# Kernel tuning notes

Hardware: AMD Instinct MI355X
Metric: run time of the kernel (lower is better)

## Reference

```python
import jax, jax.numpy as jnp
import numpy as np

B, C, H, W = 4, 128, 256, 256
N, NPOS, KS = 4000, 8, 3
CH = 2 * NPOS  # mask=False -> 2*n_pos offset channels


def setup_inputs() -> dict:
    key = jax.random.key(0)
    ks = jax.random.split(key, 8)
    x = jax.random.normal(ks[0], (B, C, H, W), jnp.float32)
    keypoints = jax.random.uniform(ks[1], (B, N, 2), jnp.float32) * 2.0 - 1.0  # [-1,1]
    w1 = jax.random.normal(ks[2], (CH, C, KS, KS), jnp.float32) * 0.05  # offset conv 3x3
    b1 = jnp.zeros((CH,), jnp.float32)
    w2 = jax.random.normal(ks[3], (CH, CH), jnp.float32) * 0.05        # offset conv 1x1
    b2 = jnp.zeros((CH,), jnp.float32)
    wsf = jax.random.normal(ks[4], (C, C), jnp.float32) * 0.05         # sf_conv 1x1 no bias
    agg_weights = jax.random.uniform(ks[5], (NPOS, C, C), jnp.float32)  # torch.rand init
    return {"x": x, "keypoints": keypoints, "w1": w1, "b1": b1, "w2": w2,
            "b2": b2, "wsf": wsf, "agg_weights": agg_weights}


def _bilinear_sample(img, px, py):
    """grid_sample(mode=bilinear, align_corners=True, padding=zeros) at pixel coords.
    img: (C,H,W); px,py: (M,). Returns (C,M)."""
    c, h, w = img.shape
    x0f = jnp.floor(px); y0f = jnp.floor(py)
    x0 = x0f.astype(jnp.int32); y0 = y0f.astype(jnp.int32)
    wx1 = px - x0f; wx0 = 1.0 - wx1
    wy1 = py - y0f; wy0 = 1.0 - wy1

    def tap(xi, yi, wgt):
        valid = ((xi >= 0) & (xi < w) & (yi >= 0) & (yi < h)).astype(img.dtype)
        v = img[:, jnp.clip(yi, 0, h - 1), jnp.clip(xi, 0, w - 1)]  # (C,M)
        return v * (wgt * valid)

    return (tap(x0, y0, wx0 * wy0) + tap(x0 + 1, y0, wx1 * wy0)
            + tap(x0, y0 + 1, wx0 * wy1) + tap(x0 + 1, y0 + 1, wx1 * wy1))


def _per_image(xi, kpts, w1, b1, w2, b2, wsf, agg_weights):
    wh = jnp.array([W - 1.0, H - 1.0], xi.dtype)
    max_offset = max(H, W) / 4.0
    kwh = (kpts / 2.0 + 0.5) * wh                      # (N,2) pixel coords, >=0
    rc = kwh.astype(jnp.int32)                          # .long() trunc (positive)
    corner = jnp.trunc(rc.astype(jnp.float32) - KS / 2.0 + 1.0).astype(jnp.int32)
    cx = jnp.clip(corner[:, 0], 0, W - 1 - KS)
    cy = jnp.clip(corner[:, 1], 0, H - 1 - KS)
    ar = jnp.arange(KS)
    # patch[n,c,a,b] = xi[c, cy_n+a, cx_n+b]
    patch = xi[:, (cy[:, None] + ar)[:, :, None], (cx[:, None] + ar)[:, None, :]]  # (C,N,KS,KS)
    patch = patch.transpose(1, 0, 2, 3)                 # (N,C,KS,KS)
    # offset network: 3x3 conv (valid) on 3x3 patch == full contraction, then ReLU, 1x1 conv
    h1 = jax.nn.relu(jnp.einsum('nchw,ochw->no', patch, w1) + b1)
    off = jnp.clip(h1 @ w2.T + b2, -max_offset, max_offset)  # (N, 2*NPOS)
    off = off.reshape(-1, 2, NPOS).transpose(0, 2, 1)        # (N,NPOS,2)
    # deform sampling positions; torch normalizes then grid_sample(align_corners=True)
    # maps exactly back to pixel coords, so sample at pixel coords directly
    pos = kwh[:, None, :] + off                              # (N,NPOS,2)
    feats = _bilinear_sample(xi, pos[..., 0].reshape(-1), pos[..., 1].reshape(-1))  # (C,N*NPOS)
    feats = feats.reshape(C, -1, NPOS).transpose(1, 0, 2)    # (N,C,NPOS)
    feats = jax.nn.selu(jnp.einsum('ncp,dc->ndp', feats, wsf))
    descs = jnp.einsum('ncp,pcd->nd', feats, agg_weights)    # (N,C)
    descs = descs / jnp.maximum(jnp.linalg.norm(descs, axis=1, keepdims=True), 1e-12)
    return descs, off


def reference(x, keypoints, w1, b1, w2, b2, wsf, agg_weights):
    f = jax.vmap(lambda xi, k: _per_image(xi, k, w1, b1, w2, b2, wsf, agg_weights))
    descriptors, offsets = f(x, keypoints)
    return descriptors, offsets  # (B,N,C), (B,N,NPOS,2)
```

## Files before the change

### kernel.cpp

```cpp
#include <hip/hip_runtime.h>
#include <math.h>

#define BB 4
#define CC 128
#define HH 256
#define WW 256
#define NN 4000
#define NPOS 8
#define KS 3
#define HWSZ (HH*WW)

#define SELU_ALPHA 1.6732632423543772f
#define SELU_SCALE 1.0507009873554805f
#define MAX_OFFSET 64.0f

typedef unsigned short ushort_t;
typedef short short8 __attribute__((ext_vector_type(8)));
typedef float f32x4 __attribute__((ext_vector_type(4)));
typedef unsigned short ushort4_t __attribute__((ext_vector_type(4)));
typedef unsigned short ushort8_t __attribute__((ext_vector_type(8)));

#define XT_ELEMS    ((size_t)BB*HH*WW*CC)
#define WSFBF_ELEMS ((size_t)CC*CC)
#define AGGT_ELEMS  ((size_t)NPOS*CC*CC)
#define W1T_ELEMS   ((size_t)16*CC*9)
#define NKP         (BB*NN)
#define NSORTBLK    ((NKP + 255) / 256)
#define HISTU_ELEMS ((size_t)NSORTBLK*256)
#define WS_NEEDED   ((XT_ELEMS+WSFBF_ELEMS+AGGT_ELEMS+W1T_ELEMS+HISTU_ELEMS)*sizeof(ushort_t) \
                     + (2*(size_t)NKP)*sizeof(int))

__device__ __forceinline__ ushort_t f2bf(float f) {
    unsigned u = __builtin_bit_cast(unsigned, f);
    unsigned r = (u + 0x7FFFu + ((u >> 16) & 1u)) >> 16;
    return (ushort_t)r;
}
__device__ __forceinline__ float bf2f(ushort_t u) {
    return __builtin_bit_cast(float, ((unsigned)u) << 16);
}

__device__ __forceinline__ int kp_bucket(const float* __restrict__ kpts, int i) {
    float kx = kpts[(size_t)i * 2 + 0];
    float ky = kpts[(size_t)i * 2 + 1];
    float kwx = (kx * 0.5f + 0.5f) * (float)(WW - 1);
    float kwy = (ky * 0.5f + 0.5f) * (float)(HH - 1);
    int rcx = (int)kwx, rcy = (int)kwy;
    int b = i / NN;
    return b * 64 + ((rcy >> 5) << 3) + (rcx >> 5);
}

__global__ __launch_bounds__(256) void ksort_hist(
    const float* __restrict__ kpts, int* __restrict__ bucket_of,
    ushort_t* __restrict__ hist63u)
{
    const int t  = threadIdx.x;
    const int hb = blockIdx.x;
    __shared__ int lh[256];
    lh[t] = 0;
    __syncthreads();
    int i = hb * 256 + t;
    if (i < NKP) {
        int bk = kp_bucket(kpts, i);
        int rank = atomicAdd(&lh[bk], 1);
        bucket_of[i] = (bk << 8) | rank;
    }
    __syncthreads();
    hist63u[hb * 256 + t] = (ushort_t)lh[t];
}

__global__ __launch_bounds__(256) void ksort_scatter(
    const int* __restrict__ bucket_of, const ushort_t* __restrict__ hist63u,
    int* __restrict__ perm)
{
    const int t = threadIdx.x;
    const int j = blockIdx.x;
    __shared__ ushort_t hall[NSORTBLK * 256];
    __shared__ int si[768];

    const int* src = (const int*)hist63u;
    int* dst = (int*)hall;
    for (int v = t; v < (NSORTBLK * 256) / 2; v += 256) dst[v] = src[v];
    __syncthreads();

    int tot = 0, before = 0;
    #pragma unroll
    for (int b2 = 0; b2 < NSORTBLK; ++b2) {
        int h = hall[b2 * 256 + t];
        tot += h;
        if (b2 < j) before += h;
    }
    si[t] = tot;
    __syncthreads();
    #pragma unroll
    for (int off = 1; off < 256; off <<= 1) {
        int add = (t >= off) ? si[t - off] : 0;
        __syncthreads();
        si[t] += add;
        __syncthreads();
    }
    int sb_t = si[t] - tot;
    __syncthreads();
    si[256 + t] = sb_t;
    si[512 + t] = before;
    __syncthreads();
    int i = j * 256 + t;
    if (i < NKP) {
        int v = bucket_of[i];
        int bk = v >> 8, rank = v & 255;
        perm[si[256 + bk] + si[512 + bk] + rank] = i;
    }
}

__global__ __launch_bounds__(256) void k0p(
    const float* __restrict__ x, ushort_t* __restrict__ xt,
    const float* __restrict__ wsf, const float* __restrict__ agg,
    const float* __restrict__ w1,
    ushort_t* __restrict__ wsf_bf, ushort_t* __restrict__ aggT_bf,
    ushort_t* __restrict__ w1t_bf)
{
    int blk = blockIdx.x;
    const int t = threadIdx.x;
    if (blk >= BB * HH * 4) {
        int i = (blk - BB * HH * 4) * 256 + t;
        if (i < CC * CC) wsf_bf[i] = f2bf(wsf[i]);
        if (i < NPOS * CC * CC) {
            int p = i >> 14, d = (i >> 7) & 127, c = i & 127;
            aggT_bf[i] = f2bf(agg[(p << 14) + (c << 7) + d]);
        }
        if (i < 16 * 1152) {
            int o = i / 1152, e = i - o * 1152, k = e >> 7, c = e & 127;
            w1t_bf[i] = f2bf(w1[o * 1152 + c * 9 + k]);
        }
        return;
    }
    int xc = blk & 3, y = (blk >> 2) & 255, b = blk >> 10;
    int x0 = xc * 64;
    __shared__ ushort_t lds[64][136];

    const float* xb = x + (size_t)b * CC * HWSZ + (size_t)y * WW + x0;
    for (int v = t; v < 2048; v += 256) {
        int c = v >> 4, xo4 = v & 15;
        float4 val = *(const float4*)(xb + (size_t)c * HWSZ + xo4 * 4);
        lds[xo4*4+0][c] = f2bf(val.x);
        lds[xo4*4+1][c] = f2bf(val.y);
        lds[xo4*4+2][c] = f2bf(val.z);
        lds[xo4*4+3][c] = f2bf(val.w);
    }
    __syncthreads();
    ushort_t* outb = xt + ((size_t)b * HWSZ + (size_t)y * WW + x0) * CC;
    for (int v = t; v < 2048; v += 256) {
        int xo = v >> 5, c4 = v & 31;
        ushort4_t val;
        val[0] = lds[xo][c4*4+0];
        val[1] = lds[xo][c4*4+1];
        val[2] = lds[xo][c4*4+2];
        val[3] = lds[xo][c4*4+3];
        *(ushort4_t*)(outb + (size_t)xo * CC + c4 * 4) = val;
    }
}

__global__ __launch_bounds__(256, 2) void k14_fused(
    const ushort_t* __restrict__ xt, const float* __restrict__ kpts,
    const ushort_t* __restrict__ w1t_bf, const float* __restrict__ b1,
    const float* __restrict__ w2, const float* __restrict__ b2,
    const ushort_t* __restrict__ wsf_bf, const ushort_t* __restrict__ aggT_bf,
    const int* __restrict__ perm,
    float* __restrict__ out_desc, float* __restrict__ out_off)
{
    const int t    = threadIdx.x;
    const int wv   = t >> 6;
    const int lane = t & 63;
    const int m    = lane & 15;
    const int q    = lane >> 4;
    const int bid  = blockIdx.x;
    const int sb   = (bid & 7) * ((BB * NN / 16) >> 3) + (bid >> 3);
    const int n0   = sb * 16;

    __shared__ ushort_t fg[CC * CC];
    union PT {
        float partials[4][16][16];
        struct { int tapoff[128][4]; float tapw[128][4]; } tp;
    };
    __shared__ PT    upt;
    __shared__ float h1f[16][17];
    __shared__ float offs[16][16];
    __shared__ float kw[16][2];
    __shared__ int   cxy[16][2];
    __shared__ int   kpi[16];
    __shared__ float wsum[4][16];
    __shared__ float rn[16];

    if (t < 16) {
        int kidx = perm[n0 + t];
        kpi[t] = kidx;
        float kx = kpts[(size_t)kidx * 2 + 0];
        float ky = kpts[(size_t)kidx * 2 + 1];
        float kwx = (kx * 0.5f + 0.5f) * (float)(WW - 1);
        float kwy = (ky * 0.5f + 0.5f) * (float)(HH - 1);
        kw[t][0] = kwx; kw[t][1] = kwy;
        int rcx = (int)kwx, rcy = (int)kwy;
        int cx = (int)truncf((float)rcx - 0.5f);
        int cy = (int)truncf((float)rcy - 0.5f);
        cxy[t][0] = min(max(cx, 0), WW - 1 - KS);
        cxy[t][1] = min(max(cy, 0), HH - 1 - KS);
    }
    __syncthreads();
    const int b = kpi[0] / NN;
    const ushort_t* xb = xt + (size_t)b * HWSZ * CC;

    {
        int px0 = cxy[m][0], py0 = cxy[m][1];
        const ushort_t* brow = w1t_bf + m * 1152 + wv * 288 + q * 8;
        short8 a0, a1, a2, a3, a4, a5, a6, a7, a8;
        #define LOAD_A(idx, dst) { \
            int e = wv * 288 + (idx) * 32 + q * 8; \
            int k = e >> 7, c = e & 127; \
            int kd = k / 3, kx2 = k - kd * 3; \
            dst = *(const short8*)(xb + ((size_t)((py0 + kd) * WW + px0 + kx2)) * CC + c); }
        LOAD_A(0, a0) LOAD_A(1, a1) LOAD_A(2, a2) LOAD_A(3, a3) LOAD_A(4, a4)
        LOAD_A(5, a5) LOAD_A(6, a6) LOAD_A(7, a7) LOAD_A(8, a8)
        #undef LOAD_A
        f32x4 hacc = {0.f, 0.f, 0.f, 0.f};
        #define MF(idx, areg) { \
            short8 bfr = *(const short8*)(brow + (idx) * 32); \
            hacc = __builtin_amdgcn_mfma_f32_16x16x32_bf16(areg, bfr, hacc, 0, 0, 0); }
        MF(0, a0) MF(1, a1) MF(2, a2) MF(3, a3) MF(4, a4)
        MF(5, a5) MF(6, a6) MF(7, a7) MF(8, a8)
        #undef MF
        #pragma unroll
        for (int r = 0; r < 4; ++r) upt.partials[wv][q * 4 + r][m] = hacc[r];
    }
    __syncthreads();
    {
        int kp = t >> 4, o = t & 15;
        float h = upt.partials[0][kp][o] + upt.partials[1][kp][o]
                + upt.partials[2][kp][o] + upt.partials[3][kp][o] + b1[o];
        h1f[kp][o] = fmaxf(h, 0.f);
    }
    __syncthreads();
    {
        int kp = t >> 4, j = t & 15;
        float s = b2[j];
        #pragma unroll
        for (int o = 0; o < 16; ++o) s += h1f[kp][o] * w2[j * 16 + o];
        s = fminf(fmaxf(s, -MAX_OFFSET), MAX_OFFSET);
        offs[kp][j] = s;
        int p = j & 7, comp = j >> 3;
        out_off[((size_t)kpi[kp] * 8 + p) * 2 + comp] = s;
    }
    __syncthreads();

    if (t < 128) {
        int kp = t >> 3, p = t & 7;
        float px = kw[kp][0] + offs[kp][p];
        float py = kw[kp][1] + offs[kp][8 + p];
        float x0f = floorf(px), y0f = floorf(py);
        int x0 = (int)x0f, y0 = (int)y0f;
        float wx1 = px - x0f, wx0 = 1.f - wx1;
        float wy1 = py - y0f, wy0 = 1.f - wy1;
        int x0c = min(max(x0, 0), WW - 1);
        int x1c = min(max(x0 + 1, 0), WW - 1);
        int y0c = min(max(y0, 0), HH - 1);
        int y1c = min(max(y0 + 1, 0), HH - 1);
        float vx0 = (x0 >= 0 && x0 < WW) ? 1.f : 0.f;
        float vx1 = (x0 + 1 >= 0 && x0 + 1 < WW) ? 1.f : 0.f;
        float vy0 = (y0 >= 0 && y0 < HH) ? 1.f : 0.f;
        float vy1 = (y0 + 1 >= 0 && y0 + 1 < HH) ? 1.f : 0.f;
        upt.tp.tapoff[t][0] = (y0c * WW + x0c) * CC;
        upt.tp.tapoff[t][1] = (y0c * WW + x1c) * CC;
        upt.tp.tapoff[t][2] = (y1c * WW + x0c) * CC;
        upt.tp.tapoff[t][3] = (y1c * WW + x1c) * CC;
        upt.tp.tapw[t][0] = wx0 * wy0 * vx0 * vy0;
        upt.tp.tapw[t][1] = wx1 * wy0 * vx1 * vy0;
        upt.tp.tapw[t][2] = wx0 * wy1 * vx0 * vy1;
        upt.tp.tapw[t][3] = wx1 * wy1 * vx1 * vy1;
    }
    __syncthreads();

    {
        const int grp = t >> 4;
        const int cl  = t & 15;
        #pragma unroll
        for (int half = 0; half < 2; ++half) {
            ushort8_t tv0[4], tv1[4], tv2[4], tv3[4];
            float4 twv[4];
            #pragma unroll
            for (int i = 0; i < 4; ++i) {
                int pair = (half * 4 + i) * 16 + grp;
                const int* to = upt.tp.tapoff[pair];
                twv[i] = *(const float4*)upt.tp.tapw[pair];
                tv0[i] = *(const ushort8_t*)(xb + to[0] + cl * 8);
                tv1[i] = *(const ushort8_t*)(xb + to[1] + cl * 8);
                tv2[i] = *(const ushort8_t*)(xb + to[2] + cl * 8);
                tv3[i] = *(const ushort8_t*)(xb + to[3] + cl * 8);
            }
            #pragma unroll
            for (int i = 0; i < 4; ++i) {
                int pair = (half * 4 + i) * 16 + grp;
                float w00 = twv[i].x, w01 = twv[i].y, w10 = twv[i].z, w11 = twv[i].w;
                ushort8_t out;
                #pragma unroll
                for (int j = 0; j < 8; ++j) {
                    float v = bf2f(tv0[i][j]) * w00;
                    v += bf2f(tv1[i][j]) * w01;
                    v += bf2f(tv2[i][j]) * w10;
                    v += bf2f(tv3[i][j]) * w11;
                    out[j] = f2bf(v);
                }
                unsigned byte = ((unsigned)(pair * 256 + cl * 16))
                              ^ (((unsigned)(pair & 7)) << 4);
                *(ushort8_t*)((char*)fg + byte) = out;
            }
        }
    }
    __syncthreads();

    for (int rti = 0; rti < 2; ++rti) {
        int rt = wv * 2 + rti;
        int r  = rt * 16 + m;
        unsigned key = ((unsigned)(r & 7)) << 4;
        short8 afr[4];
        #pragma unroll
        for (int kk = 0; kk < 4; ++kk) {
            unsigned byte = ((unsigned)(r * 256 + q * 16 + kk * 64)) ^ key;
            afr[kk] = *(const short8*)((const char*)fg + byte);
        }
        for (int ct = 0; ct < 8; ++ct) {
            const ushort_t* brow = wsf_bf + (ct * 16 + m) * CC + q * 8;
            f32x4 acc = {0.f, 0.f, 0.f, 0.f};
            #pragma unroll
            for (int kk = 0; kk < 4; ++kk) {
                short8 bfr = *(const short8*)(brow + kk * 32);
                acc = __builtin_amdgcn_mfma_f32_16x16x32_bf16(afr[kk], bfr, acc, 0, 0, 0);
            }
            #pragma unroll
            for (int rr = 0; rr < 4; ++rr) {
                float s = acc[rr];
                s = (s > 0.f) ? (SELU_SCALE * s)
                              : (SELU_SCALE * SELU_ALPHA * (expf(s) - 1.f));
                int row = rt * 16 + q * 4 + rr;
                int col = ct * 16 + m;
                unsigned byte = ((unsigned)(row * 256 + col * 2))
                              ^ (((unsigned)((row >> 3) & 7)) << 4);
                *(ushort_t*)((char*)fg + byte) = f2bf(s);
            }
        }
    }
    __syncthreads();

    f32x4 acc2[2];
    acc2[0] = (f32x4){0.f, 0.f, 0.f, 0.f};
    acc2[1] = (f32x4){0.f, 0.f, 0.f, 0.f};
    const int ctbase = wv * 2;
    for (int kk = 0; kk < 32; ++kk) {
        int p    = kk >> 2;
        int rowA = m * 8 + p;
        unsigned byte = ((unsigned)(rowA * 256 + (kk & 3) * 64 + q * 16))
                      ^ (((unsigned)((rowA >> 3) & 7)) << 4);
        short8 afr = *(const short8*)((const char*)fg + byte);
        #pragma unroll
        for (int i = 0; i < 2; ++i) {
            int ct = ctbase + i;
            const ushort_t* brow = aggT_bf + (size_t)(p * CC + ct * 16 + m) * CC
                                 + (kk & 3) * 32 + q * 8;
            short8 bfr = *(const short8*)brow;
            acc2[i] = __builtin_amdgcn_mfma_f32_16x16x32_bf16(afr, bfr, acc2[i], 0, 0, 0);
        }
    }

    {
        float ss[4];
        #pragma unroll
        for (int rr = 0; rr < 4; ++rr)
            ss[rr] = acc2[0][rr] * acc2[0][rr] + acc2[1][rr] * acc2[1][rr];
        #pragma unroll
        for (int mask = 1; mask <= 8; mask <<= 1) {
            #pragma unroll
            for (int rr = 0; rr < 4; ++rr) ss[rr] += __shfl_xor(ss[rr], mask);
        }
        if (m == 0) {
            #pragma unroll
            for (int rr = 0; rr < 4; ++rr) wsum[wv][q * 4 + rr] = ss[rr];
        }
    }
    __syncthreads();
    if (t < 16) {
        float tot = wsum[0][t] + wsum[1][t] + wsum[2][t] + wsum[3][t];
        rn[t] = 1.0f / fmaxf(sqrtf(tot), 1e-12f);
    }
    __syncthreads();
    {
        #pragma unroll
        for (int i = 0; i < 2; ++i) {
            int col = (ctbase + i) * 16 + m;
            #pragma unroll
            for (int rr = 0; rr < 4; ++rr) {
                int n = q * 4 + rr;
                out_desc[(size_t)kpi[n] * CC + col] = acc2[i][rr] * rn[n];
            }
        }
    }
}

__global__ __launch_bounds__(256, 4) void sddh_baseline(
    const float* __restrict__ x, const float* __restrict__ keypoints,
    const float* __restrict__ w1, const float* __restrict__ b1,
    const float* __restrict__ w2, const float* __restrict__ b2,
    const float* __restrict__ wsf, const float* __restrict__ agg,
    float* __restrict__ out_desc, float* __restrict__ out_off)
{
    const int bn = blockIdx.x;
    const int b  = bn / NN;
    const int t  = threadIdx.x;
    const float* xi = x + (size_t)b * CC * HWSZ;

    __shared__ float patch[CC * 9];
    __shared__ float conv_part[16][17];
    __shared__ float h1s[16];
    __shared__ float offs[16];
    __shared__ float feats[CC][NPOS];
    __shared__ float cpart2[CC][NPOS];
    __shared__ float g[CC][NPOS];
    __shared__ float dpart[CC];
    __shared__ float desc[CC];
    __shared__ float sq[128];
    __shared__ float kxy[2];

    if (t == 0) {
        float kx = keypoints[(size_t)bn * 2 + 0];
        float ky = keypoints[(size_t)bn * 2 + 1];
        kxy[0] = (kx * 0.5f + 0.5f) * (float)(WW - 1);
        kxy[1] = (ky * 0.5f + 0.5f) * (float)(HH - 1);
    }
    __syncthreads();
    const float kwx = kxy[0], kwy = kxy[1];
    const int rcx = (int)kwx, rcy = (int)kwy;
    int cx = (int)truncf((float)rcx - 0.5f);
    int cy = (int)truncf((float)rcy - 0.5f);
    cx = min(max(cx, 0), WW - 1 - KS);
    cy = min(max(cy, 0), HH - 1 - KS);

    for (int e = t; e < CC * 9; e += 256) {
        int c = e / 9, k = e % 9;
        int dy = k / 3, dx = k % 3;
        patch[e] = xi[(size_t)c * HWSZ + (cy + dy) * WW + (cx + dx)];
    }
    __syncthreads();
    {
        int o = t & 15, j = t >> 4;
        float acc = 0.f;
        const float* wo = w1 + o * (CC * 9);
        for (int e = j; e < CC * 9; e += 16) acc += patch[e] * wo[e];
        conv_part[o][j] = acc;
    }
    __syncthreads();
    if (t < 16) {
        float s = b1[t];
        #pragma unroll
        for (int j = 0; j < 16; j++) s += conv_part[t][j];
        h1s[t] = fmaxf(s, 0.f);
    }
    __syncthreads();
    if (t < 16) {
        float s = b2[t];
        #pragma unroll
        for (int k = 0; k < 16; k++) s += h1s[k] * w2[t * 16 + k];
        s = fminf(fmaxf(s, -MAX_OFFSET), MAX_OFFSET);
        offs[t] = s;
        int idx = (t < 8) ? (bn * 16 + t * 2) : (bn * 16 + (t - 8) * 2 + 1);
        out_off[idx] = s;
    }
    __syncthreads();

    for (int e = t; e < CC * NPOS; e += 256) {
        int c = e & 127, p = e >> 7;
        float px = kwx + offs[p];
        float py = kwy + offs[8 + p];
        float x0f = floorf(px), y0f = floorf(py);
        int x0 = (int)x0f, y0 = (int)y0f;
        float wx1 = px - x0f, wx0 = 1.f - wx1;
        float wy1 = py - y0f, wy0 = 1.f - wy1;
        const float* xc = xi + (size_t)c * HWSZ;
        int x0c = min(max(x0, 0), WW - 1);
        int x1c = min(max(x0 + 1, 0), WW - 1);
        int y0c = min(max(y0, 0), HH - 1);
        int y1c = min(max(y0 + 1, 0), HH - 1);
        float vx0 = (x0 >= 0 && x0 < WW) ? 1.f : 0.f;
        float vx1 = (x0 + 1 >= 0 && x0 + 1 < WW) ? 1.f : 0.f;
        float vy0 = (y0 >= 0 && y0 < HH) ? 1.f : 0.f;
        float vy1 = (y0 + 1 >= 0 && y0 + 1 < HH) ? 1.f : 0.f;
        float v = 0.f;
        v += xc[y0c * WW + x0c] * (wx0 * wy0) * (vx0 * vy0);
        v += xc[y0c * WW + x1c] * (wx1 * wy0) * (vx1 * vy0);
        v += xc[y1c * WW + x0c] * (wx0 * wy1) * (vx0 * vy1);
        v += xc[y1c * WW + x1c] * (wx1 * wy1) * (vx1 * vy1);
        feats[c][p] = v;
    }
    __syncthreads();
    {
        int d = t & 127, chalf = t >> 7;
        float acc[NPOS];
        #pragma unroll
        for (int p = 0; p < NPOS; p++) acc[p] = 0.f;
        const float* wrow = wsf + d * CC;
        int c0 = chalf * 64;
        for (int c = c0; c < c0 + 64; c++) {
            float wv = wrow[c];
            #pragma unroll
            for (int p = 0; p < NPOS; p++) acc[p] += feats[c][p] * wv;
        }
        if (chalf) {
            #pragma unroll
            for (int p = 0; p < NPOS; p++) cpart2[d][p] = acc[p];
        }
        __syncthreads();
        if (!chalf) {
            #pragma unroll
            for (int p = 0; p < NPOS; p++) {
                float s = acc[p] + cpart2[d][p];
                s = (s > 0.f) ? (SELU_SCALE * s)
                              : (SELU_SCALE * SELU_ALPHA * (expf(s) - 1.f));
                g[d][p] = s;
            }
        }
    }
    __syncthreads();
    {
        int d = t & 127, half = t >> 7;
        float acc = 0.f;
        int p0 = half * 4;
        for (int p = p0; p < p0 + 4; p++) {
            const float* ap = agg + (size_t)p * CC * CC;
            for (int e = 0; e < CC; e++) acc += g[e][p] * ap[e * CC + d];
        }
        if (half) dpart[d] = acc;
        __syncthreads();
        if (!half) {
            float v = acc + dpart[d];
            desc[d] = v;
            sq[d] = v * v;
        }
    }
    __syncthreads();
    if (t < 64) sq[t] += sq[t + 64]; __syncthreads();
    if (t < 32) sq[t] += sq[t + 32]; __syncthreads();
    if (t < 16) sq[t] += sq[t + 16]; __syncthreads();
    if (t < 8)  sq[t] += sq[t + 8];  __syncthreads();
    if (t < 4)  sq[t] += sq[t + 4];  __syncthreads();
    if (t < 2)  sq[t] += sq[t + 2];  __syncthreads();
    if (t == 0) sq[0] = fmaxf(sqrtf(sq[0] + sq[1]), 1e-12f);
    __syncthreads();
    if (t < 128) out_desc[(size_t)bn * CC + t] = desc[t] / sq[0];
}

extern "C" void kernel_launch(void* const* d_in, const int* in_sizes, int n_in,
                              void* d_out, int out_size, void* d_ws, size_t ws_size,
                              hipStream_t stream) {
    const float* x    = (const float*)d_in[0];
    const float* kpts = (const float*)d_in[1];
    const float* w1   = (const float*)d_in[2];
    const float* b1   = (const float*)d_in[3];
    const float* w2   = (const float*)d_in[4];
    const float* b2   = (const float*)d_in[5];
    const float* wsf  = (const float*)d_in[6];
    const float* agg  = (const float*)d_in[7];

    float* out_desc = (float*)d_out;
    float* out_off  = (float*)d_out + (size_t)BB * NN * CC;

    if (ws_size < WS_NEEDED) {
        hipLaunchKernelGGL(sddh_baseline, dim3(BB * NN), dim3(256), 0, stream,
                           x, kpts, w1, b1, w2, b2, wsf, agg, out_desc, out_off);
        return;
    }

    ushort_t* xt        = (ushort_t*)d_ws;
    ushort_t* wsf_bf    = xt + XT_ELEMS;
    ushort_t* aggT_bf   = wsf_bf + WSFBF_ELEMS;
    ushort_t* w1t_bf    = aggT_bf + AGGT_ELEMS;
    int*      perm      = (int*)(w1t_bf + W1T_ELEMS);
    int*      bucket_of = perm + NKP;
    ushort_t* hist63u   = (ushort_t*)(bucket_of + NKP);

    hipLaunchKernelGGL(ksort_hist, dim3(NSORTBLK), dim3(256), 0, stream,
                       kpts, bucket_of, hist63u);
    hipLaunchKernelGGL(k0p, dim3(BB * HH * 4 + 512), dim3(256), 0, stream,
                       x, xt, wsf, agg, w1, wsf_bf, aggT_bf, w1t_bf);
    hipLaunchKernelGGL(ksort_scatter, dim3(NSORTBLK), dim3(256), 0, stream,
                       bucket_of, hist63u, perm);
    hipLaunchKernelGGL(k14_fused, dim3(BB * NN / 16), dim3(256), 0, stream,
                       xt, kpts, w1t_bf, b1, w2, b2, wsf_bf, aggT_bf, perm,
                       out_desc, out_off);
}
```

Measured before the change: 113.3 us.

## Fold keypoint sort histogram into prep kernel and scatter into fused kernel

Removes the two standalone sort kernels. The histogram step now runs as extra blocks of the transpose/convert prep kernel. Each fused-kernel block recomputes the full prefix scan and scans all keypoints to find its own 16 sorted entries, which cuts two launches from the sequence. In exchange every one of the 1000 blocks redoes the scan and reads all 16000 bucket entries, adding redundant per-block work and several barriers before the main compute starts.

```diff
diff --git a/kernel.cpp b/kernel.cpp
--- a/kernel.cpp
+++ b/kernel.cpp
@@ -28,7 +28,7 @@
 #define NSORTBLK    ((NKP + 255) / 256)
 #define HISTU_ELEMS ((size_t)NSORTBLK*256)
 #define WS_NEEDED   ((XT_ELEMS+WSFBF_ELEMS+AGGT_ELEMS+W1T_ELEMS+HISTU_ELEMS)*sizeof(ushort_t) \
-                     + (2*(size_t)NKP)*sizeof(int))
+                     + (size_t)NKP*sizeof(int))
 
 __device__ __forceinline__ ushort_t f2bf(float f) {
     unsigned u = __builtin_bit_cast(unsigned, f);
@@ -49,77 +49,32 @@
     return b * 64 + ((rcy >> 5) << 3) + (rcx >> 5);
 }
 
-__global__ __launch_bounds__(256) void ksort_hist(
-    const float* __restrict__ kpts, int* __restrict__ bucket_of,
-    ushort_t* __restrict__ hist63u)
-{
-    const int t  = threadIdx.x;
-    const int hb = blockIdx.x;
-    __shared__ int lh[256];
-    lh[t] = 0;
-    __syncthreads();
-    int i = hb * 256 + t;
-    if (i < NKP) {
-        int bk = kp_bucket(kpts, i);
-        int rank = atomicAdd(&lh[bk], 1);
-        bucket_of[i] = (bk << 8) | rank;
-    }
-    __syncthreads();
-    hist63u[hb * 256 + t] = (ushort_t)lh[t];
-}
-
-__global__ __launch_bounds__(256) void ksort_scatter(
-    const int* __restrict__ bucket_of, const ushort_t* __restrict__ hist63u,
-    int* __restrict__ perm)
-{
-    const int t = threadIdx.x;
-    const int j = blockIdx.x;
-    __shared__ ushort_t hall[NSORTBLK * 256];
-    __shared__ int si[768];
-
-    const int* src = (const int*)hist63u;
-    int* dst = (int*)hall;
-    for (int v = t; v < (NSORTBLK * 256) / 2; v += 256) dst[v] = src[v];
-    __syncthreads();
-
-    int tot = 0, before = 0;
-    #pragma unroll
-    for (int b2 = 0; b2 < NSORTBLK; ++b2) {
-        int h = hall[b2 * 256 + t];
-        tot += h;
-        if (b2 < j) before += h;
-    }
-    si[t] = tot;
-    __syncthreads();
-    #pragma unroll
-    for (int off = 1; off < 256; off <<= 1) {
-        int add = (t >= off) ? si[t - off] : 0;
-        __syncthreads();
-        si[t] += add;
-        __syncthreads();
-    }
-    int sb_t = si[t] - tot;
-    __syncthreads();
-    si[256 + t] = sb_t;
-    si[512 + t] = before;
-    __syncthreads();
-    int i = j * 256 + t;
-    if (i < NKP) {
-        int v = bucket_of[i];
-        int bk = v >> 8, rank = v & 255;
-        perm[si[256 + bk] + si[512 + bk] + rank] = i;
-    }
-}
-
 __global__ __launch_bounds__(256) void k0p(
     const float* __restrict__ x, ushort_t* __restrict__ xt,
     const float* __restrict__ wsf, const float* __restrict__ agg,
-    const float* __restrict__ w1,
+    const float* __restrict__ w1, const float* __restrict__ kpts,
     ushort_t* __restrict__ wsf_bf, ushort_t* __restrict__ aggT_bf,
-    ushort_t* __restrict__ w1t_bf)
+    ushort_t* __restrict__ w1t_bf, int* __restrict__ bucket_of,
+    ushort_t* __restrict__ hist63u)
 {
     int blk = blockIdx.x;
     const int t = threadIdx.x;
+
+    if (blk >= BB * HH * 4 + 512) {
+        const int hb = blk - (BB * HH * 4 + 512);
+        __shared__ int lh[256];
+        lh[t] = 0;
+        __syncthreads();
+        int i = hb * 256 + t;
+        if (i < NKP) {
+            int bk = kp_bucket(kpts, i);
+            int rank = atomicAdd(&lh[bk], 1);
+            bucket_of[i] = (bk << 8) | rank;
+        }
+        __syncthreads();
+        hist63u[hb * 256 + t] = (ushort_t)lh[t];
+        return;
+    }
     if (blk >= BB * HH * 4) {
         int i = (blk - BB * HH * 4) * 256 + t;
         if (i < CC * CC) wsf_bf[i] = f2bf(wsf[i]);
@@ -164,7 +119,7 @@
     const ushort_t* __restrict__ w1t_bf, const float* __restrict__ b1,
     const float* __restrict__ w2, const float* __restrict__ b2,
     const ushort_t* __restrict__ wsf_bf, const ushort_t* __restrict__ aggT_bf,
-    const int* __restrict__ perm,
+    const int* __restrict__ bucket_of, const ushort_t* __restrict__ hist63u,
     float* __restrict__ out_desc, float* __restrict__ out_off)
 {
     const int t    = threadIdx.x;
@@ -174,10 +129,10 @@
     const int q    = lane >> 4;
     const int bid  = blockIdx.x;
     const int sb   = (bid & 7) * ((BB * NN / 16) >> 3) + (bid >> 3);
-    const int n0   = sb * 16;
 
     __shared__ ushort_t fg[CC * CC];
     union PT {
+        int   si[512];
         float partials[4][16][16];
         struct { int tapoff[128][4]; float tapw[128][4]; } tp;
     };
@@ -190,9 +145,46 @@
     __shared__ float wsum[4][16];
     __shared__ float rn[16];
 
+    {
+        ushort_t* hall = fg;
+        {
+            const int* src = (const int*)hist63u;
+            int* dst = (int*)hall;
+            for (int v = t; v < (NSORTBLK * 256) / 2; v += 256) dst[v] = src[v];
+        }
+        __syncthreads();
+        int run = 0;
+        #pragma unroll
+        for (int b2 = 0; b2 < NSORTBLK; ++b2) {
+            int h = hall[b2 * 256 + t];
+            hall[b2 * 256 + t] = (ushort_t)run;
+            run += h;
+        }
+        upt.si[t] = run;
+        __syncthreads();
+        #pragma unroll
+        for (int off = 1; off < 256; off <<= 1) {
+            int add = (t >= off) ? upt.si[t - off] : 0;
+            __syncthreads();
+            upt.si[t] += add;
+            __syncthreads();
+        }
+        int sb_excl = upt.si[t] - run;
+        __syncthreads();
+        upt.si[256 + t] = sb_excl;
+        __syncthreads();
+        for (int i = t; i < NKP; i += 256) {
+            int v = bucket_of[i];
+            int bk = v >> 8, rank = v & 255;
+            int j = i >> 8;
+            int pos = upt.si[256 + bk] + (int)hall[j * 256 + bk] + rank;
+            if ((pos >> 4) == sb) kpi[pos & 15] = i;
+        }
+        __syncthreads();
+    }
+
     if (t < 16) {
-        int kidx = perm[n0 + t];
-        kpi[t] = kidx;
+        int kidx = kpi[t];
         float kx = kpts[(size_t)kidx * 2 + 0];
         float ky = kpts[(size_t)kidx * 2 + 1];
         float kwx = (kx * 0.5f + 0.5f) * (float)(WW - 1);
@@ -578,17 +570,13 @@
     ushort_t* wsf_bf    = xt + XT_ELEMS;
     ushort_t* aggT_bf   = wsf_bf + WSFBF_ELEMS;
     ushort_t* w1t_bf    = aggT_bf + AGGT_ELEMS;
-    int*      perm      = (int*)(w1t_bf + W1T_ELEMS);
-    int*      bucket_of = perm + NKP;
+    int*      bucket_of = (int*)(w1t_bf + W1T_ELEMS);
     ushort_t* hist63u   = (ushort_t*)(bucket_of + NKP);
 
-    hipLaunchKernelGGL(ksort_hist, dim3(NSORTBLK), dim3(256), 0, stream,
-                       kpts, bucket_of, hist63u);
-    hipLaunchKernelGGL(k0p, dim3(BB * HH * 4 + 512), dim3(256), 0, stream,
-                       x, xt, wsf, agg, w1, wsf_bf, aggT_bf, w1t_bf);
-    hipLaunchKernelGGL(ksort_scatter, dim3(NSORTBLK), dim3(256), 0, stream,
-                       bucket_of, hist63u, perm);
+    hipLaunchKernelGGL(k0p, dim3(BB * HH * 4 + 512 + NSORTBLK), dim3(256), 0, stream,
+                       x, xt, wsf, agg, w1, kpts, wsf_bf, aggT_bf, w1t_bf,
+                       bucket_of, hist63u);
     hipLaunchKernelGGL(k14_fused, dim3(BB * NN / 16), dim3(256), 0, stream,
-                       xt, kpts, w1t_bf, b1, w2, b2, wsf_bf, aggT_bf, perm,
-                       out_desc, out_off);
-}
+                       xt, kpts, w1t_bf, b1, w2, b2, wsf_bf, aggT_bf,
+                       bucket_of, hist63u, out_desc, out_off);
+}
```

Result: slower. 128.6 us (+13.5%).
